# Kernel tuning notes

Hardware: AMD Instinct MI355X
Metric: run time of the kernel (lower is better)

The kernel has to match this reference:

```python
import jax, jax.numpy as jnp
import numpy as np

B = 2048
DIMS = [4096, 8192, 8192, 4096]
SPARSITY = 1e-4


def setup_inputs() -> dict:
    key = jax.random.key(0)
    ks = jax.random.split(key, 10)
    x = jax.random.normal(ks[0], (B, DIMS[0]), dtype=jnp.float32)
    inp = {"x": x}
    for i in range(3):
        fan_in, fan_out = DIMS[i], DIMS[i + 1]
        # xavier_uniform_ for tanh
        limit = float(np.sqrt(6.0 / (fan_in + fan_out)))
        W = jax.random.uniform(ks[1 + 3 * i], (fan_out, fan_in),
                               dtype=jnp.float32, minval=-limit, maxval=limit)
        b = jax.random.uniform(ks[2 + 3 * i], (fan_out,), dtype=jnp.float32,
                               minval=-1.0 / np.sqrt(fan_in), maxval=1.0 / np.sqrt(fan_in))
        m = jax.random.bernoulli(ks[3 + 3 * i], p=SPARSITY, shape=(fan_out, fan_in))
        inp[f"W{i+1}"] = W
        inp[f"b{i+1}"] = b
        inp[f"m{i+1}"] = m
    return inp


def reference(x, W1, b1, m1, W2, b2, m2, W3, b3, m3):
    # Each layer: mask weight, dense linear (y = x @ (W*m)^T + b), tanh except last.
    h = jnp.tanh(x @ (W1 * m1).T + b1)        # [B, 8192]
    h = jnp.tanh(h @ (W2 * m2).T + b2)        # [B, 8192]
    out = h @ (W3 * m3).T + b3                # [B, 4096]
    return out
```

## Files before the change

kernel.cpp:

```cpp
#include <hip/hip_runtime.h>
#include <stdint.h>

#define CAP 32

typedef unsigned int u32x4 __attribute__((ext_vector_type(4)));

static constexpr int BATCH = 2048;
static constexpr int D0 = 4096, D1 = 8192, D2 = 8192, D3 = 4096;
static constexpr int RP = 8192;

static constexpr size_t PREFIX_BYTES = 16u << 20;

static constexpr size_t OFF_DET   = 0;
static constexpr size_t OFF_REFD2 = 256;
static constexpr size_t ZERO_BYTES= OFF_REFD2 + (size_t)RP * 4;
static constexpr size_t OFF_CNT   = ZERO_BYTES;
static constexpr size_t OFF_TB    = OFF_CNT + 3ull * RP * 4;
static constexpr size_t OFF_RK    = OFF_TB + 2ull * RP * 4;
static constexpr size_t OFF_RW    = OFF_RK + 3ull * RP * CAP * 4;
static constexpr size_t OFF_XT    = OFF_RW + 3ull * RP * CAP * 4;
static constexpr size_t OFF_H1    = OFF_XT + (size_t)D0 * BATCH * 4;
static constexpr size_t OFF_H2    = OFF_H1 + (size_t)D1 * BATCH * 4;
static constexpr size_t WS_BIG    = OFF_H2 + (size_t)D2 * BATCH * 4;

__device__ __forceinline__ u32x4 ntload4(const u32x4* p) {
    return __builtin_nontemporal_load(p);
}

__global__ void detect_kernel(const uint8_t* __restrict__ m, unsigned* __restrict__ det) {
    const u32x4* p = (const u32x4*)m;
    const int n16 = (int)(PREFIX_BYTES / 16);
    unsigned c123 = 0, c4 = 0;
    for (int i = blockIdx.x * blockDim.x + threadIdx.x; i < n16; i += gridDim.x * blockDim.x) {
        u32x4 q = ntload4(p + i);
        if ((q.x | q.y | q.z | q.w) == 0u) continue;
        unsigned w4[4] = {q.x, q.y, q.z, q.w};
        for (int t = 0; t < 4; ++t) {
            unsigned v = w4[t];
            if (!v) continue;
            for (int bb = 0; bb < 4; ++bb) {
                if ((v >> (8 * bb)) & 0xFFu) {
                    int pm8 = (t * 4 + bb) & 7;
                    if (pm8 & 3) c123++;
                    else if (pm8 == 4) c4++;
                }
            }
        }
    }
    if (c123) atomicAdd(&det[0], c123);
    if (c4)   atomicAdd(&det[1], c4);
}

__device__ __forceinline__ int decide_mode(const unsigned* det) {
    unsigned c123 = det[0], c4 = det[1];
    if (c123 > 1050u) return 0;
    if (c123 > 400u)  return 1;
    return (c4 > 80u) ? 1 : 2;
}

template<int FAN>
__device__ __forceinline__ void extract_row(const void* mask, const float* W,
                                            int row, int mode,
                                            int* cnt, int* rowk, float* roww,
                                            int* refd_prev) {
    __shared__ int lcnt;
    __shared__ int lk[CAP];
    if (threadIdx.x == 0) lcnt = 0;
    __syncthreads();

    auto push = [&](int k) {
        int pos = atomicAdd(&lcnt, 1);
        if (pos < CAP) lk[pos] = k;
    };

    if (mode == 1) {
        constexpr int NI = FAN / 4 / 256;
        const u32x4* p = (const u32x4*)((const int*)mask + (size_t)row * FAN) + threadIdx.x;
        u32x4 v[NI];
        #pragma unroll
        for (int it = 0; it < NI; ++it) v[it] = ntload4(p + it * 256);
        #pragma unroll
        for (int it = 0; it < NI; ++it) {
            if ((v[it].x | v[it].y | v[it].z | v[it].w) == 0u) continue;
            int base = (threadIdx.x + it * 256) * 4;
            if (v[it].x) push(base + 0);
            if (v[it].y) push(base + 1);
            if (v[it].z) push(base + 2);
            if (v[it].w) push(base + 3);
        }
    } else if (mode == 0) {
        constexpr int NI = FAN / 16 / 256 ? FAN / 16 / 256 : 1;
        const u32x4* p = (const u32x4*)((const uint8_t*)mask + (size_t)row * FAN) + threadIdx.x;
        constexpr int NCH = FAN / 16;
        u32x4 v[NI];
        #pragma unroll
        for (int it = 0; it < NI; ++it)
            if (threadIdx.x + it * 256 < NCH) v[it] = ntload4(p + it * 256);
        #pragma unroll
        for (int it = 0; it < NI; ++it) {
            if (threadIdx.x + it * 256 >= NCH) continue;
            if ((v[it].x | v[it].y | v[it].z | v[it].w) == 0u) continue;
            unsigned w4[4] = {v[it].x, v[it].y, v[it].z, v[it].w};
            int base = (threadIdx.x + it * 256) * 16;
            for (int t = 0; t < 4; ++t) {
                unsigned x = w4[t];
                if (!x) continue;
                for (int bb = 0; bb < 4; ++bb)
                    if ((x >> (8 * bb)) & 0xFFu) push(base + t * 4 + bb);
            }
        }
    } else {
        constexpr int NI = FAN / 2 / 256;
        const u32x4* p = (const u32x4*)((const long long*)mask + (size_t)row * FAN) + threadIdx.x;
        u32x4 v[NI];
        #pragma unroll
        for (int it = 0; it < NI; ++it) v[it] = ntload4(p + it * 256);
        #pragma unroll
        for (int it = 0; it < NI; ++it) {
            if ((v[it].x | v[it].y | v[it].z | v[it].w) == 0u) continue;
            int base = (threadIdx.x + it * 256) * 2;
            if (v[it].x | v[it].y) push(base + 0);
            if (v[it].z | v[it].w) push(base + 1);
        }
    }
    __syncthreads();

    if (threadIdx.x == 0) {
        int c = lcnt;
        if (c > CAP) c = CAP;
        for (int a = 1; a < c; ++a) {
            int v = lk[a];
            int b = a - 1;
            while (b >= 0 && lk[b] > v) { lk[b + 1] = lk[b]; --b; }
            lk[b + 1] = v;
        }
        cnt[row] = c;
        for (int a = 0; a < c; ++a) {
            int k = lk[a];
            rowk[(size_t)row * CAP + a] = k;
            roww[(size_t)row * CAP + a] = W[(size_t)row * FAN + k];
            if (refd_prev) atomicOr(&refd_prev[k], 1);
        }
    }
}

template<bool HAS_TB, bool USE_REFD>
__device__ __forceinline__ void layer_row(int j, const float* __restrict__ inT,
                                          const float* __restrict__ bias,
                                          const float* __restrict__ tb_in,
                                          const int* __restrict__ cnt_in,
                                          const int* __restrict__ cnt,
                                          const int* __restrict__ rowk,
                                          const float* __restrict__ roww,
                                          const int* __restrict__ refd,
                                          float* __restrict__ outT) {
    const int c = cnt[j];
    if (c == 0) return;
    if (USE_REFD) { if (refd[j] == 0) return; }

    const int*   kk = rowk + (size_t)j * CAP;
    const float* ww = roww + (size_t)j * CAP;

    float base = bias[j];
    if (HAS_TB) {
        for (int e = 0; e < c; ++e) {
            int k = kk[e];
            if (cnt_in[k] == 0) base += ww[e] * tb_in[k];
        }
    }

    const int l = threadIdx.x;
    float4 acc0 = make_float4(base, base, base, base);
    float4 acc1 = acc0;

    for (int e = 0; e < c; ++e) {
        int k = kk[e];
        if (HAS_TB && cnt_in[k] == 0) continue;
        const float w = ww[e];
        const float* row = inT + (size_t)k * BATCH;
        float4 v0 = *(const float4*)(row + l * 4);
        float4 v1 = *(const float4*)(row + 1024 + l * 4);
        acc0.x += w * v0.x; acc0.y += w * v0.y; acc0.z += w * v0.z; acc0.w += w * v0.w;
        acc1.x += w * v1.x; acc1.y += w * v1.y; acc1.z += w * v1.z; acc1.w += w * v1.w;
    }

    acc0.x = tanhf(acc0.x); acc0.y = tanhf(acc0.y);
    acc0.z = tanhf(acc0.z); acc0.w = tanhf(acc0.w);
    acc1.x = tanhf(acc1.x); acc1.y = tanhf(acc1.y);
    acc1.z = tanhf(acc1.z); acc1.w = tanhf(acc1.w);

    float* orow = outT + (size_t)j * BATCH;
    *(float4*)(orow + l * 4) = acc0;
    *(float4*)(orow + 1024 + l * 4) = acc1;
}

__global__ __launch_bounds__(256) void k1_kernel(const void* __restrict__ m1, const float* __restrict__ W1,
                          const float* __restrict__ x,
                          const float* __restrict__ b1, const float* __restrict__ b2,
                          const unsigned* __restrict__ det,
                          int* __restrict__ cnt1, int* __restrict__ rk1, float* __restrict__ rw1,
                          float* __restrict__ tb1, float* __restrict__ tb2,
                          float* __restrict__ xT) {
    const int bid = blockIdx.x;
    if (bid < D1) {
        extract_row<D0>(m1, W1, bid, decide_mode(det), cnt1, rk1, rw1, nullptr);
    } else if (bid < D1 + (D0 / 32) * (BATCH / 32)) {
        __shared__ float tile[32][33];
        const int t = bid - D1;
        const int cx = t & 127;
        const int ry = t >> 7;
        const int tx = threadIdx.x & 31, ty = threadIdx.x >> 5;
        const int c0 = cx * 32, r0 = ry * 32;
        for (int i = ty; i < 32; i += 8)
            tile[i][tx] = __builtin_nontemporal_load(&x[(size_t)(r0 + i) * D0 + c0 + tx]);
        __syncthreads();
        for (int i = ty; i < 32; i += 8)
            xT[(size_t)(c0 + i) * BATCH + r0 + tx] = tile[tx][i];
    } else {
        int tid = (bid - D1 - (D0 / 32) * (BATCH / 32)) * 256 + threadIdx.x;
        if (tid < D1) tb1[tid] = tanhf(b1[tid]);
        else if (tid < D1 + D2) tb2[tid - D1] = tanhf(b2[tid - D1]);
    }
}

__global__ __launch_bounds__(256) void k2_kernel(const void* __restrict__ m2, const float* __restrict__ W2,
                          const void* __restrict__ m3, const float* __restrict__ W3,
                          const unsigned* __restrict__ det,
                          int* __restrict__ cnt2, int* __restrict__ rk2, float* __restrict__ rw2,
                          int* __restrict__ cnt3, int* __restrict__ rk3, float* __restrict__ rw3,
                          int* __restrict__ refd2,
                          const float* __restrict__ xT, const float* __restrict__ b1,
                          const int* __restrict__ cnt1, const int* __restrict__ rk1,
                          const float* __restrict__ rw1,
                          float* __restrict__ h1T) {
    const int bid = blockIdx.x;
    if (bid < D2) {
        extract_row<D1>(m2, W2, bid, decide_mode(det), cnt2, rk2, rw2, nullptr);
    } else if (bid < D2 + D3) {
        extract_row<D2>(m3, W3, bid - D2, decide_mode(det), cnt3, rk3, rw3, refd2);
    } else {
        layer_row<false, false>(bid - D2 - D3, xT, b1, nullptr, nullptr,
                                cnt1, rk1, rw1, nullptr, h1T);
    }
}

__global__ __launch_bounds__(256) void layer2_kernel(const float* __restrict__ h1T, const float* __restrict__ b2,
                              const float* __restrict__ tb1, const int* __restrict__ cnt1,
                              const int* __restrict__ cnt2, const int* __restrict__ rk2,
                              const float* __restrict__ rw2, const int* __restrict__ refd2,
                              float* __restrict__ h2T) {
    layer_row<true, true>(blockIdx.x, h1T, b2, tb1, cnt1, cnt2, rk2, rw2, refd2, h2T);
}

__global__ void l3t_kernel(const float* __restrict__ h2T,
                           const float* __restrict__ b3, const float* __restrict__ tb2,
                           const int* __restrict__ cnt2,
                           const int* __restrict__ c3, const int* __restrict__ k3,
                           const float* __restrict__ w3,
                           float* __restrict__ out) {
    __shared__ float tile[32][33];
    const int j0 = blockIdx.x * 32, b0 = blockIdx.y * 32;
    const int tx = threadIdx.x, ty = threadIdx.y;

    for (int s = 0; s < 4; ++s) {
        int jl = ty + 8 * s;
        int j = j0 + jl;
        float acc = b3[j];
        int c = c3[j];
        const int* kk = k3 + (size_t)j * CAP;
        const float* ww = w3 + (size_t)j * CAP;
        for (int e = 0; e < c; ++e) {
            int k = kk[e];
            float w = ww[e];
            acc += w * (cnt2[k] ? h2T[(size_t)k * BATCH + b0 + tx] : tb2[k]);
        }
        tile[jl][tx] = acc;
    }
    __syncthreads();
    for (int s = 0; s < 4; ++s) {
        int bl = ty + 8 * s;
        out[(size_t)(b0 + bl) * D3 + j0 + tx] = tile[tx][bl];
    }
}

template<int FAN>
__global__ void extract_only_kernel(const void* __restrict__ mask, const float* __restrict__ W,
                                    int* __restrict__ cnt, int* __restrict__ rowk,
                                    float* __restrict__ roww, const unsigned* __restrict__ det) {
    extract_row<FAN>(mask, W, blockIdx.x, decide_mode(det), cnt, rowk, roww, nullptr);
}

__global__ void out_kernel(const float* __restrict__ x,
                           const float* __restrict__ b1, const float* __restrict__ b2,
                           const float* __restrict__ b3,
                           const int* __restrict__ c1, const int* __restrict__ k1,
                           const float* __restrict__ w1,
                           const int* __restrict__ c2, const int* __restrict__ k2,
                           const float* __restrict__ w2,
                           const int* __restrict__ c3, const int* __restrict__ k3,
                           const float* __restrict__ w3,
                           float* __restrict__ out) {
    int idx = blockIdx.x * blockDim.x + threadIdx.x;
    if (idx >= BATCH * D3) return;
    int b = idx >> 12;
    int j = idx & 4095;

    float acc = b3[j];
    int c = c3[j];
    for (int e = 0; e < c; ++e) {
        int kk2 = k3[(size_t)j * CAP + e];
        float a2 = b2[kk2];
        int cc2 = c2[kk2];
        for (int e2 = 0; e2 < cc2; ++e2) {
            int kk1 = k2[(size_t)kk2 * CAP + e2];
            float a1 = b1[kk1];
            int cc1 = c1[kk1];
            for (int e1 = 0; e1 < cc1; ++e1) {
                int kk0 = k1[(size_t)kk1 * CAP + e1];
                a1 += w1[(size_t)kk1 * CAP + e1] * x[(size_t)b * D0 + kk0];
            }
            a2 += w2[(size_t)kk2 * CAP + e2] * tanhf(a1);
        }
        acc += w3[(size_t)j * CAP + e] * tanhf(a2);
    }
    out[idx] = acc;
}

extern "C" void kernel_launch(void* const* d_in, const int* in_sizes, int n_in,
                              void* d_out, int out_size, void* d_ws, size_t ws_size,
                              hipStream_t stream) {
    const float* x  = (const float*)d_in[0];
    const float* W1 = (const float*)d_in[1];
    const float* b1 = (const float*)d_in[2];
    const void*  m1 = d_in[3];
    const float* W2 = (const float*)d_in[4];
    const float* b2 = (const float*)d_in[5];
    const void*  m2 = d_in[6];
    const float* W3 = (const float*)d_in[7];
    const float* b3 = (const float*)d_in[8];
    const void*  m3 = d_in[9];

    uint8_t* ws = (uint8_t*)d_ws;
    unsigned* det = (unsigned*)(ws + OFF_DET);
    int* refd2 = (int*)(ws + OFF_REFD2);
    int* cnt1 = (int*)(ws + OFF_CNT);
    int* cnt2 = cnt1 + RP;
    int* cnt3 = cnt2 + RP;
    float* tb1 = (float*)(ws + OFF_TB);
    float* tb2 = tb1 + RP;
    int* rk1 = (int*)(ws + OFF_RK);
    int* rk2 = rk1 + (size_t)RP * CAP;
    int* rk3 = rk2 + (size_t)RP * CAP;
    float* rw1 = (float*)(ws + OFF_RW);
    float* rw2 = rw1 + (size_t)RP * CAP;
    float* rw3 = rw2 + (size_t)RP * CAP;
    float* xT  = (float*)(ws + OFF_XT);
    float* h1T = (float*)(ws + OFF_H1);
    float* h2T = (float*)(ws + OFF_H2);

    hipMemsetAsync(ws, 0, ZERO_BYTES, stream);
    detect_kernel<<<1024, 256, 0, stream>>>((const uint8_t*)m1, det);

    if (ws_size >= WS_BIG) {
        const int K1_BLOCKS = D1 + (D0 / 32) * (BATCH / 32) + (D1 + D2) / 256;
        k1_kernel<<<K1_BLOCKS, 256, 0, stream>>>(
            m1, W1, x, b1, b2, det, cnt1, rk1, rw1, tb1, tb2, xT);

        const int K2_BLOCKS = D2 + D3 + D1;
        k2_kernel<<<K2_BLOCKS, 256, 0, stream>>>(
            m2, W2, m3, W3, det,
            cnt2, rk2, rw2, cnt3, rk3, rw3, refd2,
            xT, b1, cnt1, rk1, rw1, h1T);

        layer2_kernel<<<D2, 256, 0, stream>>>(
            h1T, b2, tb1, cnt1, cnt2, rk2, rw2, refd2, h2T);

        l3t_kernel<<<dim3(D3 / 32, BATCH / 32), dim3(32, 8), 0, stream>>>(
            h2T, b3, tb2, cnt2, cnt3, rk3, rw3, (float*)d_out);
    } else {
        extract_only_kernel<D0><<<D1, 256, 0, stream>>>(m1, W1, cnt1, rk1, rw1, det);
        extract_only_kernel<D1><<<D2, 256, 0, stream>>>(m2, W2, cnt2, rk2, rw2, det);
        extract_only_kernel<D2><<<D3, 256, 0, stream>>>(m3, W3, cnt3, rk3, rw3, det);
        out_kernel<<<(BATCH * D3 + 255) / 256, 256, 0, stream>>>(
            x, b1, b2, b3,
            cnt1, rk1, rw1,
            cnt2, rk2, rw2,
            cnt3, rk3, rw3,
            (float*)d_out);
    }
}
```

Before: 169.3 us.

## Scan masks in flat chunks with global atomics and store hidden activations as fp16

Mask extraction changes from one block per row with shared-memory collection to flat 128KB chunks scanned by each block, which scatter nonzeros into per-row lists through global atomics. Sorting moves to the consumer or to a separate pass. Hidden activations h1 and h2 are stored as fp16 to halve their memory traffic, and the output uses nontemporal stores. The detection prefix and its thresholds are halved. fp16 activations reduce accuracy, and global atomics can contend when many nonzeros share a row.

Result: no change. 167.4 us (median of 2 runs) (-1.1%).

```diff
diff --git a/kernel.cpp b/kernel.cpp
--- a/kernel.cpp
+++ b/kernel.cpp
@@ -4,30 +4,34 @@
 #define CAP 32
 
 typedef unsigned int u32x4 __attribute__((ext_vector_type(4)));
+typedef _Float16 half8 __attribute__((ext_vector_type(8)));
 
 static constexpr int BATCH = 2048;
 static constexpr int D0 = 4096, D1 = 8192, D2 = 8192, D3 = 4096;
 static constexpr int RP = 8192;
-
-static constexpr size_t PREFIX_BYTES = 16u << 20;
+static constexpr size_t PREFIX_BYTES = 8u << 20;
+
+static constexpr int CHUNK16 = 8192;
+static constexpr int MAXC1 = 2048, MAXC2 = 4096, MAXC3 = 2048;
 
 static constexpr size_t OFF_DET   = 0;
 static constexpr size_t OFF_REFD2 = 256;
-static constexpr size_t ZERO_BYTES= OFF_REFD2 + (size_t)RP * 4;
-static constexpr size_t OFF_CNT   = ZERO_BYTES;
-static constexpr size_t OFF_TB    = OFF_CNT + 3ull * RP * 4;
+static constexpr size_t OFF_CNT   = OFF_REFD2 + (size_t)RP * 4;
+static constexpr size_t ZERO_BYTES= OFF_CNT + 3ull * RP * 4;
+static constexpr size_t OFF_TB    = ZERO_BYTES;
 static constexpr size_t OFF_RK    = OFF_TB + 2ull * RP * 4;
 static constexpr size_t OFF_RW    = OFF_RK + 3ull * RP * CAP * 4;
 static constexpr size_t OFF_XT    = OFF_RW + 3ull * RP * CAP * 4;
 static constexpr size_t OFF_H1    = OFF_XT + (size_t)D0 * BATCH * 4;
-static constexpr size_t OFF_H2    = OFF_H1 + (size_t)D1 * BATCH * 4;
-static constexpr size_t WS_BIG    = OFF_H2 + (size_t)D2 * BATCH * 4;
+static constexpr size_t OFF_H2    = OFF_H1 + (size_t)D1 * BATCH * 2;
+static constexpr size_t WS_BIG    = OFF_H2 + (size_t)D2 * BATCH * 2;
 
 __device__ __forceinline__ u32x4 ntload4(const u32x4* p) {
     return __builtin_nontemporal_load(p);
 }
 
-__global__ void detect_kernel(const uint8_t* __restrict__ m, unsigned* __restrict__ det) {
+__global__ __launch_bounds__(256) void detect_kernel(const uint8_t* __restrict__ m,
+                                                     unsigned* __restrict__ det) {
     const u32x4* p = (const u32x4*)m;
     const int n16 = (int)(PREFIX_BYTES / 16);
     unsigned c123 = 0, c4 = 0;
@@ -53,145 +57,135 @@
 
 __device__ __forceinline__ int decide_mode(const unsigned* det) {
     unsigned c123 = det[0], c4 = det[1];
-    if (c123 > 1050u) return 0;
-    if (c123 > 400u)  return 1;
-    return (c4 > 80u) ? 1 : 2;
-}
-
-template<int FAN>
-__device__ __forceinline__ void extract_row(const void* mask, const float* W,
-                                            int row, int mode,
-                                            int* cnt, int* rowk, float* roww,
-                                            int* refd_prev) {
-    __shared__ int lcnt;
-    __shared__ int lk[CAP];
-    if (threadIdx.x == 0) lcnt = 0;
-    __syncthreads();
-
-    auto push = [&](int k) {
-        int pos = atomicAdd(&lcnt, 1);
-        if (pos < CAP) lk[pos] = k;
-    };
-
-    if (mode == 1) {
-        constexpr int NI = FAN / 4 / 256;
-        const u32x4* p = (const u32x4*)((const int*)mask + (size_t)row * FAN) + threadIdx.x;
-        u32x4 v[NI];
+    if (c123 > 520u) return 0;
+    if (c123 > 200u) return 1;
+    return (c4 > 40u) ? 1 : 2;
+}
+
+__device__ __forceinline__ int esize_of(int mode) { return mode == 0 ? 1 : (mode == 1 ? 4 : 8); }
+
+__device__ __forceinline__ void scat(int e, int flog2, const float* W,
+                                     int* cnt, int* rk, float* rw, int* mark) {
+    int row = e >> flog2;
+    int col = e & ((1 << flog2) - 1);
+    int pos = atomicAdd(&cnt[row], 1);
+    if (pos < CAP) {
+        rk[(size_t)row * CAP + pos] = col;
+        rw[(size_t)row * CAP + pos] = W[(size_t)e];
+    }
+    if (mark) atomicOr(&mark[col], 1);
+}
+
+template<int FLOG2>
+__device__ __forceinline__ void scan_chunk(const void* __restrict__ mask, const float* __restrict__ W,
+                                           int chunk, int mode,
+                                           int* cnt, int* rk, float* rw, int* mark) {
+    const u32x4* q4 = (const u32x4*)mask;
+    const int base16 = chunk * CHUNK16;
+    #pragma unroll 1
+    for (int it = 0; it < 4; ++it) {
+        const u32x4* p = q4 + base16 + it * 2048 + threadIdx.x;
+        u32x4 v[8];
         #pragma unroll
-        for (int it = 0; it < NI; ++it) v[it] = ntload4(p + it * 256);
+        for (int t = 0; t < 8; ++t) v[t] = ntload4(p + t * 256);
         #pragma unroll
-        for (int it = 0; it < NI; ++it) {
-            if ((v[it].x | v[it].y | v[it].z | v[it].w) == 0u) continue;
-            int base = (threadIdx.x + it * 256) * 4;
-            if (v[it].x) push(base + 0);
-            if (v[it].y) push(base + 1);
-            if (v[it].z) push(base + 2);
-            if (v[it].w) push(base + 3);
-        }
-    } else if (mode == 0) {
-        constexpr int NI = FAN / 16 / 256 ? FAN / 16 / 256 : 1;
-        const u32x4* p = (const u32x4*)((const uint8_t*)mask + (size_t)row * FAN) + threadIdx.x;
-        constexpr int NCH = FAN / 16;
-        u32x4 v[NI];
-        #pragma unroll
-        for (int it = 0; it < NI; ++it)
-            if (threadIdx.x + it * 256 < NCH) v[it] = ntload4(p + it * 256);
-        #pragma unroll
-        for (int it = 0; it < NI; ++it) {
-            if (threadIdx.x + it * 256 >= NCH) continue;
-            if ((v[it].x | v[it].y | v[it].z | v[it].w) == 0u) continue;
-            unsigned w4[4] = {v[it].x, v[it].y, v[it].z, v[it].w};
-            int base = (threadIdx.x + it * 256) * 16;
-            for (int t = 0; t < 4; ++t) {
-                unsigned x = w4[t];
-                if (!x) continue;
-                for (int bb = 0; bb < 4; ++bb)
-                    if ((x >> (8 * bb)) & 0xFFu) push(base + t * 4 + bb);
+        for (int t = 0; t < 8; ++t) {
+            u32x4 q = v[t];
+            if ((q.x | q.y | q.z | q.w) == 0u) continue;
+            int i16 = base16 + it * 2048 + t * 256 + (int)threadIdx.x;
+            if (mode == 1) {
+                int eb = i16 << 2;
+                if (q.x) scat(eb + 0, FLOG2, W, cnt, rk, rw, mark);
+                if (q.y) scat(eb + 1, FLOG2, W, cnt, rk, rw, mark);
+                if (q.z) scat(eb + 2, FLOG2, W, cnt, rk, rw, mark);
+                if (q.w) scat(eb + 3, FLOG2, W, cnt, rk, rw, mark);
+            } else if (mode == 0) {
+                unsigned w4[4] = {q.x, q.y, q.z, q.w};
+                int eb = i16 << 4;
+                for (int tt = 0; tt < 4; ++tt) {
+                    unsigned x = w4[tt];
+                    if (!x) continue;
+                    for (int bb = 0; bb < 4; ++bb)
+                        if ((x >> (8 * bb)) & 0xFFu)
+                            scat(eb + tt * 4 + bb, FLOG2, W, cnt, rk, rw, mark);
+                }
+            } else {
+                int eb = i16 << 1;
+                if (q.x | q.y) scat(eb + 0, FLOG2, W, cnt, rk, rw, mark);
+                if (q.z | q.w) scat(eb + 1, FLOG2, W, cnt, rk, rw, mark);
             }
         }
-    } else {
-        constexpr int NI = FAN / 2 / 256;
-        const u32x4* p = (const u32x4*)((const long long*)mask + (size_t)row * FAN) + threadIdx.x;
-        u32x4 v[NI];
-        #pragma unroll
-        for (int it = 0; it < NI; ++it) v[it] = ntload4(p + it * 256);
-        #pragma unroll
-        for (int it = 0; it < NI; ++it) {
-            if ((v[it].x | v[it].y | v[it].z | v[it].w) == 0u) continue;
-            int base = (threadIdx.x + it * 256) * 2;
-            if (v[it].x | v[it].y) push(base + 0);
-            if (v[it].z | v[it].w) push(base + 1);
-        }
-    }
-    __syncthreads();
-
-    if (threadIdx.x == 0) {
-        int c = lcnt;
-        if (c > CAP) c = CAP;
-        for (int a = 1; a < c; ++a) {
-            int v = lk[a];
-            int b = a - 1;
-            while (b >= 0 && lk[b] > v) { lk[b + 1] = lk[b]; --b; }
-            lk[b + 1] = v;
-        }
-        cnt[row] = c;
-        for (int a = 0; a < c; ++a) {
-            int k = lk[a];
-            rowk[(size_t)row * CAP + a] = k;
-            roww[(size_t)row * CAP + a] = W[(size_t)row * FAN + k];
-            if (refd_prev) atomicOr(&refd_prev[k], 1);
-        }
-    }
-}
-
-template<bool HAS_TB, bool USE_REFD>
-__device__ __forceinline__ void layer_row(int j, const float* __restrict__ inT,
+    }
+}
+
+template<bool HAS_TB, bool USE_REFD, bool IN_HALF>
+__device__ __forceinline__ void layer_row(int j, const void* __restrict__ inT,
                                           const float* __restrict__ bias,
                                           const float* __restrict__ tb_in,
                                           const int* __restrict__ cnt_in,
                                           const int* __restrict__ cnt,
-                                          const int* __restrict__ rowk,
-                                          const float* __restrict__ roww,
+                                          const int* __restrict__ rk,
+                                          const float* __restrict__ rw,
                                           const int* __restrict__ refd,
-                                          float* __restrict__ outT) {
-    const int c = cnt[j];
+                                          _Float16* __restrict__ outT) {
+    int c = cnt[j]; if (c > CAP) c = CAP;
     if (c == 0) return;
-    if (USE_REFD) { if (refd[j] == 0) return; }
-
-    const int*   kk = rowk + (size_t)j * CAP;
-    const float* ww = roww + (size_t)j * CAP;
+    if (USE_REFD && refd[j] == 0) return;
+
+    __shared__ int   ci[CAP];
+    __shared__ float wv[CAP];
+    if (threadIdx.x == 0) {
+        for (int a = 0; a < c; ++a) { ci[a] = rk[(size_t)j * CAP + a]; wv[a] = rw[(size_t)j * CAP + a]; }
+        for (int a = 1; a < c; ++a) {
+            int k = ci[a]; float w = wv[a]; int b = a - 1;
+            while (b >= 0 && ci[b] > k) { ci[b + 1] = ci[b]; wv[b + 1] = wv[b]; --b; }
+            ci[b + 1] = k; wv[b + 1] = w;
+        }
+    }
+    __syncthreads();
 
     float base = bias[j];
-    if (HAS_TB) {
-        for (int e = 0; e < c; ++e) {
-            int k = kk[e];
-            if (cnt_in[k] == 0) base += ww[e] * tb_in[k];
-        }
-    }
+    if (HAS_TB)
+        for (int e = 0; e < c; ++e)
+            if (cnt_in[ci[e]] == 0) base += wv[e] * tb_in[ci[e]];
 
     const int l = threadIdx.x;
-    float4 acc0 = make_float4(base, base, base, base);
-    float4 acc1 = acc0;
+    float acc[8];
+    #pragma unroll
+    for (int i = 0; i < 8; ++i) acc[i] = base;
 
     for (int e = 0; e < c; ++e) {
-        int k = kk[e];
+        int k = ci[e];
         if (HAS_TB && cnt_in[k] == 0) continue;
-        const float w = ww[e];
-        const float* row = inT + (size_t)k * BATCH;
-        float4 v0 = *(const float4*)(row + l * 4);
-        float4 v1 = *(const float4*)(row + 1024 + l * 4);
-        acc0.x += w * v0.x; acc0.y += w * v0.y; acc0.z += w * v0.z; acc0.w += w * v0.w;
-        acc1.x += w * v1.x; acc1.y += w * v1.y; acc1.z += w * v1.z; acc1.w += w * v1.w;
-    }
-
-    acc0.x = tanhf(acc0.x); acc0.y = tanhf(acc0.y);
-    acc0.z = tanhf(acc0.z); acc0.w = tanhf(acc0.w);
-    acc1.x = tanhf(acc1.x); acc1.y = tanhf(acc1.y);
-    acc1.z = tanhf(acc1.z); acc1.w = tanhf(acc1.w);
-
-    float* orow = outT + (size_t)j * BATCH;
-    *(float4*)(orow + l * 4) = acc0;
-    *(float4*)(orow + 1024 + l * 4) = acc1;
+        float w = wv[e];
+        if (IN_HALF) {
+            half8 v = ((const half8*)((const _Float16*)inT + (size_t)k * BATCH))[l];
+            #pragma unroll
+            for (int i = 0; i < 8; ++i) acc[i] += w * (float)v[i];
+        } else {
+            const float* row = (const float*)inT + (size_t)k * BATCH + l * 8;
+            float4 v0 = *(const float4*)row;
+            float4 v1 = *(const float4*)(row + 4);
+            acc[0] += w * v0.x; acc[1] += w * v0.y; acc[2] += w * v0.z; acc[3] += w * v0.w;
+            acc[4] += w * v1.x; acc[5] += w * v1.y; acc[6] += w * v1.z; acc[7] += w * v1.w;
+        }
+    }
+
+    half8 o;
+    #pragma unroll
+    for (int i = 0; i < 8; ++i) o[i] = (_Float16)tanhf(acc[i]);
+    ((half8*)(outT + (size_t)j * BATCH))[l] = o;
+}
+
+__device__ __forceinline__ void sort_row_global(int j, const int* cnt, int* rk, float* rw) {
+    int c = cnt[j]; if (c > CAP) c = CAP;
+    if (c <= 1) return;
+    int* K = rk + (size_t)j * CAP; float* W_ = rw + (size_t)j * CAP;
+    for (int a = 1; a < c; ++a) {
+        int k = K[a]; float w = W_[a]; int b = a - 1;
+        while (b >= 0 && K[b] > k) { K[b + 1] = K[b]; W_[b + 1] = W_[b]; --b; }
+        K[b + 1] = k; W_[b + 1] = w;
+    }
 }
 
 __global__ __launch_bounds__(256) void k1_kernel(const void* __restrict__ m1, const float* __restrict__ W1,
@@ -202,13 +196,14 @@
                           float* __restrict__ tb1, float* __restrict__ tb2,
                           float* __restrict__ xT) {
     const int bid = blockIdx.x;
-    if (bid < D1) {
-        extract_row<D0>(m1, W1, bid, decide_mode(det), cnt1, rk1, rw1, nullptr);
-    } else if (bid < D1 + (D0 / 32) * (BATCH / 32)) {
+    if (bid < MAXC1) {
+        const int mode = decide_mode(det);
+        const int nc = (int)(((size_t)D1 * D0 * esize_of(mode)) >> 17);
+        if (bid < nc) scan_chunk<12>(m1, W1, bid, mode, cnt1, rk1, rw1, nullptr);
+    } else if (bid < MAXC1 + (D0 / 32) * (BATCH / 32)) {
         __shared__ float tile[32][33];
-        const int t = bid - D1;
-        const int cx = t & 127;
-        const int ry = t >> 7;
+        const int t = bid - MAXC1;
+        const int cx = t & 127, ry = t >> 7;
         const int tx = threadIdx.x & 31, ty = threadIdx.x >> 5;
         const int c0 = cx * 32, r0 = ry * 32;
         for (int i = ty; i < 32; i += 8)
@@ -217,7 +212,7 @@
         for (int i = ty; i < 32; i += 8)
             xT[(size_t)(c0 + i) * BATCH + r0 + tx] = tile[tx][i];
     } else {
-        int tid = (bid - D1 - (D0 / 32) * (BATCH / 32)) * 256 + threadIdx.x;
+        int tid = (bid - MAXC1 - (D0 / 32) * (BATCH / 32)) * 256 + threadIdx.x;
         if (tid < D1) tb1[tid] = tanhf(b1[tid]);
         else if (tid < D1 + D2) tb2[tid - D1] = tanhf(b2[tid - D1]);
     }
@@ -232,27 +227,39 @@
                           const float* __restrict__ xT, const float* __restrict__ b1,
                           const int* __restrict__ cnt1, const int* __restrict__ rk1,
                           const float* __restrict__ rw1,
-                          float* __restrict__ h1T) {
+                          _Float16* __restrict__ h1T) {
+    const int bid = blockIdx.x;
+    if (bid < MAXC2) {
+        const int mode = decide_mode(det);
+        const int nc = (int)(((size_t)D2 * D1 * esize_of(mode)) >> 17);
+        if (bid < nc) scan_chunk<13>(m2, W2, bid, mode, cnt2, rk2, rw2, nullptr);
+    } else if (bid < MAXC2 + MAXC3) {
+        const int mode = decide_mode(det);
+        const int nc = (int)(((size_t)D3 * D2 * esize_of(mode)) >> 17);
+        const int ch = bid - MAXC2;
+        if (ch < nc) scan_chunk<13>(m3, W3, ch, mode, cnt3, rk3, rw3, refd2);
+    } else {
+        layer_row<false, false, false>(bid - MAXC2 - MAXC3, xT, b1, nullptr, nullptr,
+                                       cnt1, rk1, rw1, nullptr, h1T);
+    }
+}
+
+__global__ __launch_bounds__(256) void k3_kernel(const _Float16* __restrict__ h1T, const float* __restrict__ b2,
+                          const float* __restrict__ tb1, const int* __restrict__ cnt1,
+                          const int* __restrict__ cnt2, const int* __restrict__ rk2,
+                          const float* __restrict__ rw2, const int* __restrict__ refd2,
+                          _Float16* __restrict__ h2T,
+                          const int* __restrict__ cnt3, int* __restrict__ rk3, float* __restrict__ rw3) {
     const int bid = blockIdx.x;
     if (bid < D2) {
-        extract_row<D1>(m2, W2, bid, decide_mode(det), cnt2, rk2, rw2, nullptr);
-    } else if (bid < D2 + D3) {
-        extract_row<D2>(m3, W3, bid - D2, decide_mode(det), cnt3, rk3, rw3, refd2);
+        layer_row<true, true, true>(bid, h1T, b2, tb1, cnt1, cnt2, rk2, rw2, refd2, h2T);
     } else {
-        layer_row<false, false>(bid - D2 - D3, xT, b1, nullptr, nullptr,
-                                cnt1, rk1, rw1, nullptr, h1T);
-    }
-}
-
-__global__ __launch_bounds__(256) void layer2_kernel(const float* __restrict__ h1T, const float* __restrict__ b2,
-                              const float* __restrict__ tb1, const int* __restrict__ cnt1,
-                              const int* __restrict__ cnt2, const int* __restrict__ rk2,
-                              const float* __restrict__ rw2, const int* __restrict__ refd2,
-                              float* __restrict__ h2T) {
-    layer_row<true, true>(blockIdx.x, h1T, b2, tb1, cnt1, cnt2, rk2, rw2, refd2, h2T);
-}
-
-__global__ void l3t_kernel(const float* __restrict__ h2T,
+        int j = (bid - D2) * 256 + threadIdx.x;
+        if (j < D3) sort_row_global(j, cnt3, rk3, rw3);
+    }
+}
+
+__global__ void l3t_kernel(const _Float16* __restrict__ h2T,
                            const float* __restrict__ b3, const float* __restrict__ tb2,
                            const int* __restrict__ cnt2,
                            const int* __restrict__ c3, const int* __restrict__ k3,
@@ -266,59 +273,68 @@
         int jl = ty + 8 * s;
         int j = j0 + jl;
         float acc = b3[j];
-        int c = c3[j];
+        int c = c3[j]; if (c > CAP) c = CAP;
         const int* kk = k3 + (size_t)j * CAP;
         const float* ww = w3 + (size_t)j * CAP;
         for (int e = 0; e < c; ++e) {
             int k = kk[e];
             float w = ww[e];
-            acc += w * (cnt2[k] ? h2T[(size_t)k * BATCH + b0 + tx] : tb2[k]);
+            acc += w * (cnt2[k] ? (float)h2T[(size_t)k * BATCH + b0 + tx] : tb2[k]);
         }
         tile[jl][tx] = acc;
     }
     __syncthreads();
     for (int s = 0; s < 4; ++s) {
         int bl = ty + 8 * s;
-        out[(size_t)(b0 + bl) * D3 + j0 + tx] = tile[tx][bl];
-    }
-}
-
-template<int FAN>
-__global__ void extract_only_kernel(const void* __restrict__ mask, const float* __restrict__ W,
-                                    int* __restrict__ cnt, int* __restrict__ rowk,
-                                    float* __restrict__ roww, const unsigned* __restrict__ det) {
-    extract_row<FAN>(mask, W, blockIdx.x, decide_mode(det), cnt, rowk, roww, nullptr);
+        __builtin_nontemporal_store(tile[tx][bl], &out[(size_t)(b0 + bl) * D3 + j0 + tx]);
+    }
+}
+
+__global__ __launch_bounds__(256) void scan1_kernel(const void* m, const float* W, const unsigned* det,
+                                                    int* cnt, int* rk, float* rw) {
+    const int mode = decide_mode(det);
+    const int nc = (int)(((size_t)D1 * D0 * esize_of(mode)) >> 17);
+    if (blockIdx.x < (unsigned)nc) scan_chunk<12>(m, W, blockIdx.x, mode, cnt, rk, rw, nullptr);
+}
+__global__ __launch_bounds__(256) void scan2_kernel(const void* m, const float* W, const unsigned* det,
+                                                    int* cnt, int* rk, float* rw) {
+    const int mode = decide_mode(det);
+    const int nc = (int)(((size_t)D2 * D1 * esize_of(mode)) >> 17);
+    if (blockIdx.x < (unsigned)nc) scan_chunk<13>(m, W, blockIdx.x, mode, cnt, rk, rw, nullptr);
+}
+__global__ __launch_bounds__(256) void scan3_kernel(const void* m, const float* W, const unsigned* det,
+                                                    int* cnt, int* rk, float* rw) {
+    const int mode = decide_mode(det);
+    const int nc = (int)(((size_t)D3 * D2 * esize_of(mode)) >> 17);
+    if (blockIdx.x < (unsigned)nc) scan_chunk<13>(m, W, blockIdx.x, mode, cnt, rk, rw, nullptr);
+}
+__global__ __launch_bounds__(256) void sortall_kernel(const int* cnt, int* rk, float* rw) {
+    int r = blockIdx.x * 256 + threadIdx.x;
+    if (r < 3 * RP) sort_row_global(r, cnt, rk, rw);
 }
 
 __global__ void out_kernel(const float* __restrict__ x,
                            const float* __restrict__ b1, const float* __restrict__ b2,
                            const float* __restrict__ b3,
-                           const int* __restrict__ c1, const int* __restrict__ k1,
-                           const float* __restrict__ w1,
-                           const int* __restrict__ c2, const int* __restrict__ k2,
-                           const float* __restrict__ w2,
-                           const int* __restrict__ c3, const int* __restrict__ k3,
-                           const float* __restrict__ w3,
+                           const int* __restrict__ c1, const int* __restrict__ k1, const float* __restrict__ w1,
+                           const int* __restrict__ c2, const int* __restrict__ k2, const float* __restrict__ w2,
+                           const int* __restrict__ c3, const int* __restrict__ k3, const float* __restrict__ w3,
                            float* __restrict__ out) {
     int idx = blockIdx.x * blockDim.x + threadIdx.x;
     if (idx >= BATCH * D3) return;
-    int b = idx >> 12;
-    int j = idx & 4095;
-
+    int b = idx >> 12, j = idx & 4095;
     float acc = b3[j];
-    int c = c3[j];
+    int c = c3[j]; if (c > CAP) c = CAP;
     for (int e = 0; e < c; ++e) {
         int kk2 = k3[(size_t)j * CAP + e];
         float a2 = b2[kk2];
-        int cc2 = c2[kk2];
+        int cc2 = c2[kk2]; if (cc2 > CAP) cc2 = CAP;
         for (int e2 = 0; e2 < cc2; ++e2) {
             int kk1 = k2[(size_t)kk2 * CAP + e2];
             float a1 = b1[kk1];
-            int cc1 = c1[kk1];
-            for (int e1 = 0; e1 < cc1; ++e1) {
-                int kk0 = k1[(size_t)kk1 * CAP + e1];
-                a1 += w1[(size_t)kk1 * CAP + e1] * x[(size_t)b * D0 + kk0];
-            }
+            int cc1 = c1[kk1]; if (cc1 > CAP) cc1 = CAP;
+            for (int e1 = 0; e1 < cc1; ++e1)
+                a1 += w1[(size_t)kk1 * CAP + e1] * x[(size_t)b * D0 + k1[(size_t)kk1 * CAP + e1]];
             a2 += w2[(size_t)kk2 * CAP + e2] * tanhf(a1);
         }
         acc += w3[(size_t)j * CAP + e] * tanhf(a2);
@@ -355,37 +371,36 @@
     float* rw2 = rw1 + (size_t)RP * CAP;
     float* rw3 = rw2 + (size_t)RP * CAP;
     float* xT  = (float*)(ws + OFF_XT);
-    float* h1T = (float*)(ws + OFF_H1);
-    float* h2T = (float*)(ws + OFF_H2);
+    _Float16* h1T = (_Float16*)(ws + OFF_H1);
+    _Float16* h2T = (_Float16*)(ws + OFF_H2);
 
     hipMemsetAsync(ws, 0, ZERO_BYTES, stream);
     detect_kernel<<<1024, 256, 0, stream>>>((const uint8_t*)m1, det);
 
     if (ws_size >= WS_BIG) {
-        const int K1_BLOCKS = D1 + (D0 / 32) * (BATCH / 32) + (D1 + D2) / 256;
+        const int K1_BLOCKS = MAXC1 + (D0 / 32) * (BATCH / 32) + (D1 + D2) / 256;
         k1_kernel<<<K1_BLOCKS, 256, 0, stream>>>(
             m1, W1, x, b1, b2, det, cnt1, rk1, rw1, tb1, tb2, xT);
 
-        const int K2_BLOCKS = D2 + D3 + D1;
+        const int K2_BLOCKS = MAXC2 + MAXC3 + D1;
         k2_kernel<<<K2_BLOCKS, 256, 0, stream>>>(
             m2, W2, m3, W3, det,
             cnt2, rk2, rw2, cnt3, rk3, rw3, refd2,
             xT, b1, cnt1, rk1, rw1, h1T);
 
-        layer2_kernel<<<D2, 256, 0, stream>>>(
-            h1T, b2, tb1, cnt1, cnt2, rk2, rw2, refd2, h2T);
+        k3_kernel<<<D2 + D3 / 256, 256, 0, stream>>>(
+            h1T, b2, tb1, cnt1, cnt2, rk2, rw2, refd2, h2T, cnt3, rk3, rw3);
 
         l3t_kernel<<<dim3(D3 / 32, BATCH / 32), dim3(32, 8), 0, stream>>>(
             h2T, b3, tb2, cnt2, cnt3, rk3, rw3, (float*)d_out);
     } else {
-        extract_only_kernel<D0><<<D1, 256, 0, stream>>>(m1, W1, cnt1, rk1, rw1, det);
-        extract_only_kernel<D1><<<D2, 256, 0, stream>>>(m2, W2, cnt2, rk2, rw2, det);
-        extract_only_kernel<D2><<<D3, 256, 0, stream>>>(m3, W3, cnt3, rk3, rw3, det);
+        scan1_kernel<<<MAXC1, 256, 0, stream>>>(m1, W1, det, cnt1, rk1, rw1);
+        scan2_kernel<<<MAXC2, 256, 0, stream>>>(m2, W2, det, cnt2, rk2, rw2);
+        scan3_kernel<<<MAXC3, 256, 0, stream>>>(m3, W3, det, cnt3, rk3, rw3);
+        sortall_kernel<<<3 * RP / 256, 256, 0, stream>>>(cnt1, rk1, rw1);
         out_kernel<<<(BATCH * D3 + 255) / 256, 256, 0, stream>>>(
             x, b1, b2, b3,
-            cnt1, rk1, rw1,
-            cnt2, rk2, rw2,
-            cnt3, rk3, rw3,
+            cnt1, rk1, rw1, cnt2, rk2, rw2, cnt3, rk3, rw3,
             (float*)d_out);
     }
 }
```
